# Kernel optimization log

Measured on AMD Instinct MI355X. Metric: run time of the kernel, lower is better.

The kernel has to match this reference:

```python
import jax, jax.numpy as jnp
import numpy as np

N = 100000   # nodes
E = 1600000  # edges
D = 128      # out_feats
V = 5000     # annotation_size
L = 3        # n_steps SAGE layers


def setup_inputs() -> dict:
    key = jax.random.key(0)
    k0, k1, k2, k3, k4 = jax.random.split(key, 5)
    annotation = jax.random.randint(k0, (N,), 0, V)
    src = jax.random.randint(k1, (E,), 0, N)
    dst = jax.random.randint(k2, (E,), 0, N)
    emb = jax.random.normal(k3, (V, D), dtype=jnp.float32) * 0.02
    Ws = jax.random.normal(k4, (L, D, D), dtype=jnp.float32) / np.sqrt(D).astype(np.float32)
    bs = jnp.zeros((L, D), dtype=jnp.float32)
    return {"annotation": annotation, "src": src, "dst": dst, "emb": emb, "Ws": Ws, "bs": bs}


def reference(annotation, src, dst, emb, Ws, bs):
    # tok_embedding == 2: embedding lookup of node token ids
    h = emb[annotation]                                              # [N, D]
    # in-degree per destination node (constant across layers)
    deg = jax.ops.segment_sum(jnp.ones_like(src, dtype=jnp.float32), dst, num_segments=N)
    inv = 1.0 / (deg + 1.0)                                          # [N]
    # DGL SAGEConv, aggregator_type='gcn', eval mode (feat_drop is identity):
    #   h_neigh = (h_self + sum_{u->v} h_u) / (in_deg + 1); rst = relu(h_neigh @ W + b)
    for l in range(L):
        agg = jax.ops.segment_sum(h[src], dst, num_segments=N)       # [N, D] gather-scatter
        h = jax.nn.relu(((h + agg) * inv[:, None]) @ Ws[l] + bs[l])
    # residual=False -> merged node features are just h ('_merge_on nodes h')
    return h
```

## Files before the change

### kernel.cpp

```cpp
#include <hip/hip_runtime.h>
#include <hip/hip_fp16.h>


#define D 128
#define PBLK 128
#define BSH 7

typedef float f32x4 __attribute__((ext_vector_type(4)));
typedef _Float16 f16x8 __attribute__((ext_vector_type(8)));

__global__ __launch_bounds__(256) void k_hist(
    const int* __restrict__ dst, int* __restrict__ hist,
    int E, int chunk, int nbk) {
    __shared__ int lh[1024];
    int j = blockIdx.x, tid = threadIdx.x;
    for (int i = tid; i < nbk; i += 256) lh[i] = 0;
    __syncthreads();
    int e0 = j * chunk, e1 = min(E, e0 + chunk);
    for (int e = e0 + tid; e < e1; e += 256)
        atomicAdd(&lh[dst[e] >> BSH], 1);
    __syncthreads();
    for (int i = tid; i < nbk; i += 256) hist[(size_t)j * nbk + i] = lh[i];
}

__global__ void k_scan_offs(int* __restrict__ hist, int* __restrict__ tot, int nbk) {
    __shared__ int s[PBLK];
    int b = blockIdx.x, j = threadIdx.x;
    int v = hist[(size_t)j * nbk + b];
    s[j] = v;
    __syncthreads();
    for (int off = 1; off < PBLK; off <<= 1) {
        int x = (j >= off) ? s[j - off] : 0;
        __syncthreads();
        s[j] += x;
        __syncthreads();
    }
    hist[(size_t)j * nbk + b] = s[j] - v;
    if (j == PBLK - 1) tot[b] = s[j];
}

__global__ void k_scan_tot(int* __restrict__ tot, int* __restrict__ row_ptr,
                           int nbk, int N, int E) {
    __shared__ int s[1024];
    int t = threadIdx.x;
    int v = (t < nbk) ? tot[t] : 0;
    s[t] = v;
    __syncthreads();
    for (int off = 1; off < 1024; off <<= 1) {
        int x = (t >= off) ? s[t - off] : 0;
        __syncthreads();
        s[t] += x;
        __syncthreads();
    }
    if (t < nbk) tot[t] = s[t] - v;
    if (t == 0) { tot[nbk] = E; row_ptr[N] = E; }
}

__global__ __launch_bounds__(256) void k_scatter(
    const int* __restrict__ src, const int* __restrict__ dst,
    const int* __restrict__ ann, const int* __restrict__ hist,
    const int* __restrict__ tot, int2* __restrict__ tmp,
    int E, int chunk, int nbk) {
    __shared__ int cur[1024];
    int j = blockIdx.x, tid = threadIdx.x;
    for (int i = tid; i < nbk; i += 256)
        cur[i] = tot[i] + hist[(size_t)j * nbk + i];
    __syncthreads();
    int e0 = j * chunk, e1 = min(E, e0 + chunk);
    for (int e = e0 + tid; e < e1; e += 256) {
        int d = dst[e], s = src[e];
        int p = atomicAdd(&cur[d >> BSH], 1);
        tmp[p] = make_int2(s, ((d & ((1 << BSH) - 1)) << 13) | ann[s]);
    }
}

__global__ __launch_bounds__(256) void k_place(
    const int2* __restrict__ tmp, const int* __restrict__ tot,
    int* __restrict__ row_ptr, int* __restrict__ eax, int* __restrict__ eay,
    int N) {
    __shared__ int cnt[1 << BSH], sc[1 << BSH];
    int b = blockIdx.x, tid = threadIdx.x;
    int base = tot[b], end = tot[b + 1];
    if (tid < (1 << BSH)) cnt[tid] = 0;
    __syncthreads();
    for (int i = base + tid; i < end; i += 256)
        atomicAdd(&cnt[((unsigned)tmp[i].y) >> 13], 1);
    __syncthreads();
    if (tid < (1 << BSH)) sc[tid] = cnt[tid];
    __syncthreads();
    for (int off = 1; off < (1 << BSH); off <<= 1) {
        int x = (tid < (1 << BSH) && tid >= off) ? sc[tid - off] : 0;
        __syncthreads();
        if (tid < (1 << BSH)) sc[tid] += x;
        __syncthreads();
    }
    if (tid < (1 << BSH)) {
        int excl = sc[tid] - cnt[tid];
        int d0 = (b << BSH) + tid;
        if (d0 < N) row_ptr[d0] = base + excl;
        cnt[tid] = excl;
    }
    __syncthreads();
    for (int i = base + tid; i < end; i += 256) {
        int2 w = tmp[i];
        int p = atomicAdd(&cnt[((unsigned)w.y) >> 13], 1);
        eax[base + p] = w.x;
        eay[base + p] = w.y & 0x1FFF;
    }
}

union H16Chunk { float4 f4; __half2 h2[4]; __half h[8]; };

__global__ void k_h16(const float* __restrict__ x, __half* __restrict__ y, int n8) {
    int i = blockIdx.x * blockDim.x + threadIdx.x;
    if (i >= n8) return;
    const float4* p = (const float4*)x;
    float4 a = p[2 * i], b = p[2 * i + 1];
    H16Chunk u;
    u.h2[0] = __floats2half2_rn(a.x, a.y);
    u.h2[1] = __floats2half2_rn(a.z, a.w);
    u.h2[2] = __floats2half2_rn(b.x, b.y);
    u.h2[3] = __floats2half2_rn(b.z, b.w);
    *(float4*)&y[8 * i] = u.f4;
}

__global__ void k_wfrag(const float* __restrict__ Ws, __half* __restrict__ Wf) {
    const float* W = Ws + (size_t)(blockIdx.x + 1) * D * D;
    __half* o = Wf + (size_t)blockIdx.x * 2048 * 8;
    for (int idx = threadIdx.x; idx < 2048; idx += 256) {
        int l = idx & 63, ks = (idx >> 6) & 3, nt = idx >> 8;
        int kq = (l >> 4) * 8;
        int col = nt * 16 + (l & 15);
        H16Chunk u;
        #pragma unroll
        for (int j = 0; j < 8; j++)
            u.h[j] = __float2half(W[(ks * 32 + kq + j) * 128 + col]);
        *(float4*)&o[idx * 8] = u.f4;
    }
}

#define XT_LD 136
__global__ __launch_bounds__(256) void k_gemm_mfma(
    const __half* __restrict__ x16, const float* __restrict__ W,
    __half* __restrict__ g16, int n, int ntiles) {
    __shared__ __half Bf[8 * 4 * 64 * 8];
    __shared__ __half Xt[64 * XT_LD];
    int tid = threadIdx.x;
    int lane = tid & 63;
    int wv = tid >> 6;

    for (int idx = tid; idx < 8 * 4 * 64; idx += 256) {
        int l = idx & 63, ks = (idx >> 6) & 3, nt = idx >> 8;
        int kq = (l >> 4) * 8;
        int col = nt * 16 + (l & 15);
        H16Chunk u;
        #pragma unroll
        for (int j = 0; j < 8; j++)
            u.h[j] = __float2half(W[(ks * 32 + kq + j) * 128 + col]);
        *(float4*)&Bf[idx * 8] = u.f4;
    }
    __syncthreads();

    f16x8 breg[8][4];
    #pragma unroll
    for (int nt = 0; nt < 8; nt++)
        #pragma unroll
        for (int ks = 0; ks < 4; ks++)
            breg[nt][ks] = *(f16x8*)&Bf[((nt * 4 + ks) * 64 + lane) * 8];

    int srow = tid >> 2;
    int sc = (tid & 3) * 32;
    int m = lane & 15, quad = lane >> 4;

    for (int tile = blockIdx.x; tile < ntiles; tile += gridDim.x) {
        int row0 = tile * 64;
        __syncthreads();
        {
            int gr = row0 + srow;
            if (gr >= n) gr = n - 1;
            const float4* xp = (const float4*)&x16[(size_t)gr * 128 + sc];
            float4 v0 = xp[0], v1 = xp[1], v2 = xp[2], v3 = xp[3];
            float4* xd = (float4*)&Xt[srow * XT_LD + sc];
            xd[0] = v0; xd[1] = v1; xd[2] = v2; xd[3] = v3;
        }
        __syncthreads();

        f32x4 acc[8];
        #pragma unroll
        for (int nt = 0; nt < 8; nt++) acc[nt] = (f32x4){0.f, 0.f, 0.f, 0.f};
        #pragma unroll
        for (int ks = 0; ks < 4; ks++) {
            f16x8 a = *(f16x8*)&Xt[(wv * 16 + m) * XT_LD + ks * 32 + quad * 8];
            #pragma unroll
            for (int nt = 0; nt < 8; nt++)
                acc[nt] = __builtin_amdgcn_mfma_f32_16x16x32_f16(a, breg[nt][ks], acc[nt], 0, 0, 0);
        }
        __syncthreads();
        #pragma unroll
        for (int nt = 0; nt < 8; nt++)
            #pragma unroll
            for (int r = 0; r < 4; r++)
                Xt[(wv * 16 + quad * 4 + r) * XT_LD + nt * 16 + m] = __float2half(acc[nt][r]);
        __syncthreads();
        {
            int gr = row0 + srow;
            if (gr < n) {
                float4* gp = (float4*)&g16[(size_t)gr * 128 + sc];
                float4* xs = (float4*)&Xt[srow * XT_LD + sc];
                gp[0] = xs[0]; gp[1] = xs[1]; gp[2] = xs[2]; gp[3] = xs[3];
            }
        }
    }
}

template<bool SELY>
__global__ __launch_bounds__(256, 8) void k_agg_gemm(
    const float4* __restrict__ tab, const int* __restrict__ selfidx,
    const int* __restrict__ row_ptr, const int* __restrict__ ea,
    const float4* __restrict__ bias4, const __half* __restrict__ Wf,
    __half* __restrict__ g16, int n) {
    __shared__ __half Xt[32 * XT_LD];
    __shared__ int cursor;
    int tid = threadIdx.x;
    int lane = tid & 63;
    int wv = tid >> 6;
    int g = lane >> 4;
    int q = lane & 15;
    int row0 = blockIdx.x * 32;

    if (tid == 0) cursor = 0;
    float4 b0 = bias4[2 * q], b1 = bias4[2 * q + 1];
    __syncthreads();

    #define ACCUM(raw) do { H16Chunk u; u.f4 = (raw);                          \
        float2 t0 = __half22float2(u.h2[0]); acc[0] += t0.x; acc[1] += t0.y;   \
        float2 t1 = __half22float2(u.h2[1]); acc[2] += t1.x; acc[3] += t1.y;   \
        float2 t2 = __half22float2(u.h2[2]); acc[4] += t2.x; acc[5] += t2.y;   \
        float2 t3 = __half22float2(u.h2[3]); acc[6] += t3.x; acc[7] += t3.y; } while (0)

    for (;;) {
        int r;
        if (lane == 0) r = atomicAdd(&cursor, 1);
        r = __builtin_amdgcn_readfirstlane(__shfl(r, 0, 64));
        if (r >= 32) break;
        int v = row0 + r;
        int vv = (v < n) ? v : 0;
        int beg = __builtin_amdgcn_readfirstlane(row_ptr[vv]);
        int end = (v < n) ? __builtin_amdgcn_readfirstlane(row_ptr[vv + 1]) : beg;
        int deg = end - beg;
        float acc[8] = {};
        if (g == 0) {
            int sr = SELY ? selfidx[vv] : vv;
            ACCUM(tab[(size_t)sr * 16 + q]);
        }
        int quads = deg >> 2;
        int p = 0;
        for (; p + 4 <= quads; p += 4) {
            int eb = beg + 4 * p + g;
            int x0 = ea[eb + 0], x1 = ea[eb + 4];
            int x2 = ea[eb + 8], x3 = ea[eb + 12];
            float4 r0 = tab[(size_t)x0 * 16 + q];
            float4 r1 = tab[(size_t)x1 * 16 + q];
            float4 r2 = tab[(size_t)x2 * 16 + q];
            float4 r3 = tab[(size_t)x3 * 16 + q];
            ACCUM(r0); ACCUM(r1); ACCUM(r2); ACCUM(r3);
        }
        for (; p < quads; p++) ACCUM(tab[(size_t)ea[beg + 4 * p + g] * 16 + q]);
        int tail = deg & 3;
        if (g < tail) ACCUM(tab[(size_t)ea[beg + 4 * quads + g] * 16 + q]);

        #pragma unroll
        for (int jj = 0; jj < 8; jj++) {
            acc[jj] += __shfl_down(acc[jj], 16, 64);
            acc[jj] += __shfl_down(acc[jj], 32, 64);
        }
        if (g == 0) {
            float sc = 1.0f / (float)(deg + 1);
            H16Chunk u;
            u.h2[0] = __floats2half2_rn(fmaxf(acc[0] * sc + b0.x, 0.f),
                                        fmaxf(acc[1] * sc + b0.y, 0.f));
            u.h2[1] = __floats2half2_rn(fmaxf(acc[2] * sc + b0.z, 0.f),
                                        fmaxf(acc[3] * sc + b0.w, 0.f));
            u.h2[2] = __floats2half2_rn(fmaxf(acc[4] * sc + b1.x, 0.f),
                                        fmaxf(acc[5] * sc + b1.y, 0.f));
            u.h2[3] = __floats2half2_rn(fmaxf(acc[6] * sc + b1.z, 0.f),
                                        fmaxf(acc[7] * sc + b1.w, 0.f));
            *(float4*)&Xt[r * XT_LD + q * 8] = u.f4;
        }
    }
    __syncthreads();

    int stripe = wv >> 1;
    int ntb = (wv & 1) * 4;
    f32x4 cacc[4];
    #pragma unroll
    for (int t = 0; t < 4; t++) cacc[t] = (f32x4){0.f, 0.f, 0.f, 0.f};
    #pragma unroll
    for (int ks = 0; ks < 4; ks++) {
        f16x8 a = *(f16x8*)&Xt[(stripe * 16 + q) * XT_LD + ks * 32 + g * 8];
        #pragma unroll
        for (int t = 0; t < 4; t++) {
            f16x8 b = *(const f16x8*)&Wf[(((ntb + t) * 4 + ks) * 64 + lane) * 8];
            cacc[t] = __builtin_amdgcn_mfma_f32_16x16x32_f16(a, b, cacc[t], 0, 0, 0);
        }
        __builtin_amdgcn_sched_barrier(0);
    }
    __syncthreads();
    #pragma unroll
    for (int t = 0; t < 4; t++)
        #pragma unroll
        for (int r4 = 0; r4 < 4; r4++)
            Xt[(stripe * 16 + g * 4 + r4) * XT_LD + (ntb + t) * 16 + q] =
                __float2half(cacc[t][r4]);
    __syncthreads();
    {
        int srow = tid >> 3, c = tid & 7;
        int gr = row0 + srow;
        float4 v0 = *(float4*)&Xt[srow * XT_LD + c * 16];
        float4 v1 = *(float4*)&Xt[srow * XT_LD + c * 16 + 8];
        if (gr < n) {
            float4* gp = (float4*)&g16[(size_t)gr * 128 + c * 16];
            gp[0] = v0;
            gp[1] = v1;
        }
    }
    #undef ACCUM
}

template<bool SELY, bool OUT32>
__global__ __launch_bounds__(256) void k_agg(
    const float4* __restrict__ tab, const int* __restrict__ selfidx,
    const int* __restrict__ row_ptr, const int* __restrict__ ea,
    const float4* __restrict__ bias4,
    __half* __restrict__ h16out, float* __restrict__ f32out, int n) {
    int v = blockIdx.x * 4 + (threadIdx.x >> 6);
    int lane = threadIdx.x & 63;
    int g = lane >> 4;
    int q = lane & 15;
    int beg = row_ptr[v], end = row_ptr[v + 1];
    int deg = end - beg;
    float acc[8] = {};

    #define ACCUM(raw) do { H16Chunk u; u.f4 = (raw);                          \
        float2 t0 = __half22float2(u.h2[0]); acc[0] += t0.x; acc[1] += t0.y;   \
        float2 t1 = __half22float2(u.h2[1]); acc[2] += t1.x; acc[3] += t1.y;   \
        float2 t2 = __half22float2(u.h2[2]); acc[4] += t2.x; acc[5] += t2.y;   \
        float2 t3 = __half22float2(u.h2[3]); acc[6] += t3.x; acc[7] += t3.y; } while (0)

    if (g == 0) {
        int sr = SELY ? selfidx[v] : v;
        ACCUM(tab[(size_t)sr * 16 + q]);
    }

    int quads = deg >> 2;
    int p = 0;
    for (; p + 4 <= quads; p += 4) {
        int eb = beg + 4 * p + g;
        int x0 = ea[eb + 0], x1 = ea[eb + 4], x2 = ea[eb + 8], x3 = ea[eb + 12];
        float4 r0 = tab[(size_t)x0 * 16 + q], r1 = tab[(size_t)x1 * 16 + q];
        float4 r2 = tab[(size_t)x2 * 16 + q], r3 = tab[(size_t)x3 * 16 + q];
        ACCUM(r0); ACCUM(r1); ACCUM(r2); ACCUM(r3);
    }
    for (; p < quads; p++) ACCUM(tab[(size_t)ea[beg + 4 * p + g] * 16 + q]);
    int tail = deg & 3;
    if (g < tail) ACCUM(tab[(size_t)ea[beg + 4 * quads + g] * 16 + q]);
    #undef ACCUM

    #pragma unroll
    for (int j = 0; j < 8; j++) {
        acc[j] += __shfl_down(acc[j], 16, 64);
        acc[j] += __shfl_down(acc[j], 32, 64);
    }
    if (g == 0) {
        float sc = 1.0f / (float)(deg + 1);
        float4 b0 = bias4[2 * q], b1 = bias4[2 * q + 1];
        float o[8];
        o[0] = fmaxf(acc[0] * sc + b0.x, 0.f);
        o[1] = fmaxf(acc[1] * sc + b0.y, 0.f);
        o[2] = fmaxf(acc[2] * sc + b0.z, 0.f);
        o[3] = fmaxf(acc[3] * sc + b0.w, 0.f);
        o[4] = fmaxf(acc[4] * sc + b1.x, 0.f);
        o[5] = fmaxf(acc[5] * sc + b1.y, 0.f);
        o[6] = fmaxf(acc[6] * sc + b1.z, 0.f);
        o[7] = fmaxf(acc[7] * sc + b1.w, 0.f);
        if (!OUT32) {
            H16Chunk u;
            u.h2[0] = __floats2half2_rn(o[0], o[1]);
            u.h2[1] = __floats2half2_rn(o[2], o[3]);
            u.h2[2] = __floats2half2_rn(o[4], o[5]);
            u.h2[3] = __floats2half2_rn(o[6], o[7]);
            *(float4*)&h16out[(size_t)v * 128 + q * 8] = u.f4;
        } else {
            f32x4 a = {o[0], o[1], o[2], o[3]};
            f32x4 b = {o[4], o[5], o[6], o[7]};
            __builtin_nontemporal_store(a, (f32x4*)&f32out[(size_t)v * 128 + q * 8]);
            __builtin_nontemporal_store(b, (f32x4*)&f32out[(size_t)v * 128 + q * 8 + 4]);
        }
    }
}

extern "C" void kernel_launch(void* const* d_in, const int* in_sizes, int n_in,
                              void* d_out, int out_size, void* d_ws, size_t ws_size,
                              hipStream_t stream) {
    const int*   ann = (const int*)d_in[0];
    const int*   src = (const int*)d_in[1];
    const int*   dst = (const int*)d_in[2];
    const float* emb = (const float*)d_in[3];
    const float* Ws  = (const float*)d_in[4];
    const float* bs  = (const float*)d_in[5];
    float* out = (float*)d_out;

    const int N = in_sizes[0];
    const int E = in_sizes[1];
    const int V = in_sizes[3] / D;
    const int NT32 = (N + 31) / 32;
    const int VT64 = (V + 63) / 64;
    const int NBK  = (N + (1 << BSH) - 1) >> BSH;
    const int CHK  = (E + PBLK - 1) / PBLK;

    int*  deg     = (int*)d_ws;
    int*  row_ptr = deg + N;
    int*  bsum    = row_ptr + ((N + 1 + 3) & ~3);
    int*  eax     = bsum + 512;
    int*  eay     = eax + E;
    __half* hA16  = (__half*)(eay + E);
    __half* gB16  = hA16 + (size_t)N * D;
    __half* embW16= gB16 + (size_t)N * D;
    __half* emb16 = embW16 + (size_t)V * D;
    int2* tmp  = (int2*)hA16;
    int*  hist = (int*)gB16;
    int*  tot  = hist + (size_t)PBLK * NBK;
    __half* Wf2 = (__half*)deg;
    __half* Wf3 = Wf2 + 2048 * 8;

    k_h16<<<(V * D / 8 + 255) / 256, 256, 0, stream>>>(emb, emb16, V * D / 8);
    k_wfrag<<<2, 256, 0, stream>>>(Ws, Wf2);
    k_gemm_mfma<<<VT64, 256, 0, stream>>>(emb16, Ws, embW16, V, VT64);

    k_hist<<<PBLK, 256, 0, stream>>>(dst, hist, E, CHK, NBK);
    k_scan_offs<<<NBK, PBLK, 0, stream>>>(hist, tot, NBK);
    k_scan_tot<<<1, 1024, 0, stream>>>(tot, row_ptr, NBK, N, E);
    k_scatter<<<PBLK, 256, 0, stream>>>(src, dst, ann, hist, tot, tmp, E, CHK, NBK);
    k_place<<<NBK, 256, 0, stream>>>(tmp, tot, row_ptr, eax, eay, N);

    k_agg_gemm<true><<<NT32, 256, 0, stream>>>(
        (const float4*)embW16, ann, row_ptr, eay, (const float4*)bs,
        Wf2, gB16, N);

    k_agg_gemm<false><<<NT32, 256, 0, stream>>>(
        (const float4*)gB16, nullptr, row_ptr, eax, (const float4*)(bs + D),
        Wf3, hA16, N);

    k_agg<false, true><<<N / 4, 256, 0, stream>>>(
        (const float4*)hA16, nullptr, row_ptr, eax, (const float4*)(bs + 2 * D),
        nullptr, out, N);
}
```

Measured before the change: 399.4 us.

## Merge prep kernels into one launch and fold total scan via last-block pattern

Combines the embedding fp16 conversion, the embedding GEMM, the weight fragment packing and the destination histogram into one heterogeneous kernel whose blocks branch on block index. The fp32 to fp16 conversion of emb is fused into the GEMM tile load, which removes the intermediate emb16 buffer. The separate single-block total scan is folded into the per-bucket scan kernel using an atomic counter, so the last block to finish does the global scan. This cuts kernel launches and one round trip through memory. The cost is a threadfence-based handoff and a serial chunked scan in one block.

```diff
diff --git a/kernel.cpp b/kernel.cpp
--- a/kernel.cpp
+++ b/kernel.cpp
@@ -9,22 +9,119 @@
 typedef float f32x4 __attribute__((ext_vector_type(4)));
 typedef _Float16 f16x8 __attribute__((ext_vector_type(8)));
 
-__global__ __launch_bounds__(256) void k_hist(
-    const int* __restrict__ dst, int* __restrict__ hist,
-    int E, int chunk, int nbk) {
-    __shared__ int lh[1024];
-    int j = blockIdx.x, tid = threadIdx.x;
-    for (int i = tid; i < nbk; i += 256) lh[i] = 0;
-    __syncthreads();
-    int e0 = j * chunk, e1 = min(E, e0 + chunk);
-    for (int e = e0 + tid; e < e1; e += 256)
-        atomicAdd(&lh[dst[e] >> BSH], 1);
-    __syncthreads();
-    for (int i = tid; i < nbk; i += 256) hist[(size_t)j * nbk + i] = lh[i];
-}
-
-__global__ void k_scan_offs(int* __restrict__ hist, int* __restrict__ tot, int nbk) {
+union H16Chunk { float4 f4; __half2 h2[4]; __half h[8]; };
+
+#define XT_LD 136
+
+__global__ __launch_bounds__(256) void k_prep(
+    const float* __restrict__ emb, const float* __restrict__ Ws,
+    __half* __restrict__ embW16, const int* __restrict__ dst,
+    int* __restrict__ hist, int* __restrict__ done, __half* __restrict__ Wf,
+    int V, int VT, int E, int chunk, int nbk) {
+    __shared__ __half Bf[8 * 4 * 64 * 8];
+    __shared__ __half Xt[64 * XT_LD];
+    int bid = blockIdx.x, tid = threadIdx.x;
+
+    if (bid < VT) {
+        int lane = tid & 63, wv = tid >> 6;
+        for (int idx = tid; idx < 8 * 4 * 64; idx += 256) {
+            int l = idx & 63, ks = (idx >> 6) & 3, nt = idx >> 8;
+            int kq = (l >> 4) * 8;
+            int col = nt * 16 + (l & 15);
+            H16Chunk u;
+            #pragma unroll
+            for (int j = 0; j < 8; j++)
+                u.h[j] = __float2half(Ws[(ks * 32 + kq + j) * 128 + col]);
+            *(float4*)&Bf[idx * 8] = u.f4;
+        }
+        __syncthreads();
+        f16x8 breg[8][4];
+        #pragma unroll
+        for (int nt = 0; nt < 8; nt++)
+            #pragma unroll
+            for (int ks = 0; ks < 4; ks++)
+                breg[nt][ks] = *(f16x8*)&Bf[((nt * 4 + ks) * 64 + lane) * 8];
+
+        int srow = tid >> 2;
+        int sc = (tid & 3) * 32;
+        int m = lane & 15, quad = lane >> 4;
+        int row0 = bid * 64;
+        {
+            int gr = row0 + srow;
+            if (gr >= V) gr = V - 1;
+            const float4* xp = (const float4*)&emb[(size_t)gr * 128 + sc];
+            float4* xd = (float4*)&Xt[srow * XT_LD + sc];
+            #pragma unroll
+            for (int k = 0; k < 4; k++) {
+                float4 a = xp[2 * k], b = xp[2 * k + 1];
+                H16Chunk u;
+                u.h2[0] = __floats2half2_rn(a.x, a.y);
+                u.h2[1] = __floats2half2_rn(a.z, a.w);
+                u.h2[2] = __floats2half2_rn(b.x, b.y);
+                u.h2[3] = __floats2half2_rn(b.z, b.w);
+                xd[k] = u.f4;
+            }
+        }
+        __syncthreads();
+        f32x4 acc[8];
+        #pragma unroll
+        for (int nt = 0; nt < 8; nt++) acc[nt] = (f32x4){0.f, 0.f, 0.f, 0.f};
+        #pragma unroll
+        for (int ks = 0; ks < 4; ks++) {
+            f16x8 a = *(f16x8*)&Xt[(wv * 16 + m) * XT_LD + ks * 32 + quad * 8];
+            #pragma unroll
+            for (int nt = 0; nt < 8; nt++)
+                acc[nt] = __builtin_amdgcn_mfma_f32_16x16x32_f16(a, breg[nt][ks], acc[nt], 0, 0, 0);
+        }
+        __syncthreads();
+        #pragma unroll
+        for (int nt = 0; nt < 8; nt++)
+            #pragma unroll
+            for (int r = 0; r < 4; r++)
+                Xt[(wv * 16 + quad * 4 + r) * XT_LD + nt * 16 + m] = __float2half(acc[nt][r]);
+        __syncthreads();
+        {
+            int gr = row0 + srow;
+            if (gr < V) {
+                float4* gp = (float4*)&embW16[(size_t)gr * 128 + sc];
+                float4* xs = (float4*)&Xt[srow * XT_LD + sc];
+                gp[0] = xs[0]; gp[1] = xs[1]; gp[2] = xs[2]; gp[3] = xs[3];
+            }
+        }
+    } else if (bid < VT + PBLK) {
+        int j = bid - VT;
+        int* lh = (int*)Bf;
+        for (int i = tid; i < nbk; i += 256) lh[i] = 0;
+        __syncthreads();
+        int e0 = j * chunk, e1 = min(E, e0 + chunk);
+        for (int e = e0 + tid; e < e1; e += 256)
+            atomicAdd(&lh[dst[e] >> BSH], 1);
+        __syncthreads();
+        for (int i = tid; i < nbk; i += 256) hist[(size_t)j * nbk + i] = lh[i];
+    } else if (bid < VT + PBLK + 2) {
+        int l2 = bid - VT - PBLK;
+        const float* W = Ws + (size_t)(l2 + 1) * D * D;
+        __half* o = Wf + (size_t)l2 * 2048 * 8;
+        for (int idx = tid; idx < 2048; idx += 256) {
+            int l = idx & 63, ks = (idx >> 6) & 3, nt = idx >> 8;
+            int kq = (l >> 4) * 8;
+            int col = nt * 16 + (l & 15);
+            H16Chunk u;
+            #pragma unroll
+            for (int j = 0; j < 8; j++)
+                u.h[j] = __float2half(W[(ks * 32 + kq + j) * 128 + col]);
+            *(float4*)&o[idx * 8] = u.f4;
+        }
+    } else {
+        if (tid == 0) *done = 0;
+    }
+}
+
+__global__ __launch_bounds__(PBLK) void k_scanZ(
+    int* __restrict__ hist, int* __restrict__ tot, int* __restrict__ row_ptr,
+    int* __restrict__ done, int nbk, int N, int E) {
     __shared__ int s[PBLK];
+    __shared__ int amLast;
     int b = blockIdx.x, j = threadIdx.x;
     int v = hist[(size_t)j * nbk + b];
     s[j] = v;
@@ -37,23 +134,35 @@
     }
     hist[(size_t)j * nbk + b] = s[j] - v;
     if (j == PBLK - 1) tot[b] = s[j];
-}
-
-__global__ void k_scan_tot(int* __restrict__ tot, int* __restrict__ row_ptr,
-                           int nbk, int N, int E) {
-    __shared__ int s[1024];
-    int t = threadIdx.x;
-    int v = (t < nbk) ? tot[t] : 0;
-    s[t] = v;
-    __syncthreads();
-    for (int off = 1; off < 1024; off <<= 1) {
-        int x = (t >= off) ? s[t - off] : 0;
-        __syncthreads();
-        s[t] += x;
-        __syncthreads();
-    }
-    if (t < nbk) tot[t] = s[t] - v;
-    if (t == 0) { tot[nbk] = E; row_ptr[N] = E; }
+    __threadfence();
+    __syncthreads();
+    if (j == 0) {
+        int t = atomicAdd(done, 1);
+        amLast = (t == nbk - 1);
+    }
+    __syncthreads();
+    if (amLast) {
+        __threadfence();
+        int carry = 0;
+        int chunks = (nbk + PBLK - 1) / PBLK;
+        for (int c = 0; c < chunks; c++) {
+            int idx = c * PBLK + j;
+            int val = (idx < nbk) ? tot[idx] : 0;
+            s[j] = val;
+            __syncthreads();
+            for (int off = 1; off < PBLK; off <<= 1) {
+                int x = (j >= off) ? s[j - off] : 0;
+                __syncthreads();
+                s[j] += x;
+                __syncthreads();
+            }
+            if (idx < nbk) tot[idx] = s[j] - val + carry;
+            int ctot = s[PBLK - 1];
+            __syncthreads();
+            carry += ctot;
+        }
+        if (j == 0) { tot[nbk] = E; row_ptr[N] = E; }
+    }
 }
 
 __global__ __launch_bounds__(256) void k_scatter(
@@ -106,110 +215,6 @@
         int p = atomicAdd(&cnt[((unsigned)w.y) >> 13], 1);
         eax[base + p] = w.x;
         eay[base + p] = w.y & 0x1FFF;
-    }
-}
-
-union H16Chunk { float4 f4; __half2 h2[4]; __half h[8]; };
-
-__global__ void k_h16(const float* __restrict__ x, __half* __restrict__ y, int n8) {
-    int i = blockIdx.x * blockDim.x + threadIdx.x;
-    if (i >= n8) return;
-    const float4* p = (const float4*)x;
-    float4 a = p[2 * i], b = p[2 * i + 1];
-    H16Chunk u;
-    u.h2[0] = __floats2half2_rn(a.x, a.y);
-    u.h2[1] = __floats2half2_rn(a.z, a.w);
-    u.h2[2] = __floats2half2_rn(b.x, b.y);
-    u.h2[3] = __floats2half2_rn(b.z, b.w);
-    *(float4*)&y[8 * i] = u.f4;
-}
-
-__global__ void k_wfrag(const float* __restrict__ Ws, __half* __restrict__ Wf) {
-    const float* W = Ws + (size_t)(blockIdx.x + 1) * D * D;
-    __half* o = Wf + (size_t)blockIdx.x * 2048 * 8;
-    for (int idx = threadIdx.x; idx < 2048; idx += 256) {
-        int l = idx & 63, ks = (idx >> 6) & 3, nt = idx >> 8;
-        int kq = (l >> 4) * 8;
-        int col = nt * 16 + (l & 15);
-        H16Chunk u;
-        #pragma unroll
-        for (int j = 0; j < 8; j++)
-            u.h[j] = __float2half(W[(ks * 32 + kq + j) * 128 + col]);
-        *(float4*)&o[idx * 8] = u.f4;
-    }
-}
-
-#define XT_LD 136
-__global__ __launch_bounds__(256) void k_gemm_mfma(
-    const __half* __restrict__ x16, const float* __restrict__ W,
-    __half* __restrict__ g16, int n, int ntiles) {
-    __shared__ __half Bf[8 * 4 * 64 * 8];
-    __shared__ __half Xt[64 * XT_LD];
-    int tid = threadIdx.x;
-    int lane = tid & 63;
-    int wv = tid >> 6;
-
-    for (int idx = tid; idx < 8 * 4 * 64; idx += 256) {
-        int l = idx & 63, ks = (idx >> 6) & 3, nt = idx >> 8;
-        int kq = (l >> 4) * 8;
-        int col = nt * 16 + (l & 15);
-        H16Chunk u;
-        #pragma unroll
-        for (int j = 0; j < 8; j++)
-            u.h[j] = __float2half(W[(ks * 32 + kq + j) * 128 + col]);
-        *(float4*)&Bf[idx * 8] = u.f4;
-    }
-    __syncthreads();
-
-    f16x8 breg[8][4];
-    #pragma unroll
-    for (int nt = 0; nt < 8; nt++)
-        #pragma unroll
-        for (int ks = 0; ks < 4; ks++)
-            breg[nt][ks] = *(f16x8*)&Bf[((nt * 4 + ks) * 64 + lane) * 8];
-
-    int srow = tid >> 2;
-    int sc = (tid & 3) * 32;
-    int m = lane & 15, quad = lane >> 4;
-
-    for (int tile = blockIdx.x; tile < ntiles; tile += gridDim.x) {
-        int row0 = tile * 64;
-        __syncthreads();
-        {
-            int gr = row0 + srow;
-            if (gr >= n) gr = n - 1;
-            const float4* xp = (const float4*)&x16[(size_t)gr * 128 + sc];
-            float4 v0 = xp[0], v1 = xp[1], v2 = xp[2], v3 = xp[3];
-            float4* xd = (float4*)&Xt[srow * XT_LD + sc];
-            xd[0] = v0; xd[1] = v1; xd[2] = v2; xd[3] = v3;
-        }
-        __syncthreads();
-
-        f32x4 acc[8];
-        #pragma unroll
-        for (int nt = 0; nt < 8; nt++) acc[nt] = (f32x4){0.f, 0.f, 0.f, 0.f};
-        #pragma unroll
-        for (int ks = 0; ks < 4; ks++) {
-            f16x8 a = *(f16x8*)&Xt[(wv * 16 + m) * XT_LD + ks * 32 + quad * 8];
-            #pragma unroll
-            for (int nt = 0; nt < 8; nt++)
-                acc[nt] = __builtin_amdgcn_mfma_f32_16x16x32_f16(a, breg[nt][ks], acc[nt], 0, 0, 0);
-        }
-        __syncthreads();
-        #pragma unroll
-        for (int nt = 0; nt < 8; nt++)
-            #pragma unroll
-            for (int r = 0; r < 4; r++)
-                Xt[(wv * 16 + quad * 4 + r) * XT_LD + nt * 16 + m] = __float2half(acc[nt][r]);
-        __syncthreads();
-        {
-            int gr = row0 + srow;
-            if (gr < n) {
-                float4* gp = (float4*)&g16[(size_t)gr * 128 + sc];
-                float4* xs = (float4*)&Xt[srow * XT_LD + sc];
-                gp[0] = xs[0]; gp[1] = xs[1]; gp[2] = xs[2]; gp[3] = xs[3];
-            }
-        }
     }
 }
 
@@ -426,21 +431,20 @@
     __half* hA16  = (__half*)(eay + E);
     __half* gB16  = hA16 + (size_t)N * D;
     __half* embW16= gB16 + (size_t)N * D;
-    __half* emb16 = embW16 + (size_t)V * D;
     int2* tmp  = (int2*)hA16;
     int*  hist = (int*)gB16;
     int*  tot  = hist + (size_t)PBLK * NBK;
+    int*  done = bsum;
     __half* Wf2 = (__half*)deg;
     __half* Wf3 = Wf2 + 2048 * 8;
 
-    k_h16<<<(V * D / 8 + 255) / 256, 256, 0, stream>>>(emb, emb16, V * D / 8);
-    k_wfrag<<<2, 256, 0, stream>>>(Ws, Wf2);
-    k_gemm_mfma<<<VT64, 256, 0, stream>>>(emb16, Ws, embW16, V, VT64);
-
-    k_hist<<<PBLK, 256, 0, stream>>>(dst, hist, E, CHK, NBK);
-    k_scan_offs<<<NBK, PBLK, 0, stream>>>(hist, tot, NBK);
-    k_scan_tot<<<1, 1024, 0, stream>>>(tot, row_ptr, NBK, N, E);
+    k_prep<<<VT64 + PBLK + 2 + 1, 256, 0, stream>>>(
+        emb, Ws, embW16, dst, hist, done, Wf2, V, VT64, E, CHK, NBK);
+
+    k_scanZ<<<NBK, PBLK, 0, stream>>>(hist, tot, row_ptr, done, NBK, N, E);
+
     k_scatter<<<PBLK, 256, 0, stream>>>(src, dst, ann, hist, tot, tmp, E, CHK, NBK);
+
     k_place<<<NBK, 256, 0, stream>>>(tmp, tot, row_ptr, eax, eay, N);
 
     k_agg_gemm<true><<<NT32, 256, 0, stream>>>(
```

After: 438.9 us. +9.9%, slower.
